# Optimization experiments

Measured on AMD Instinct MI355X. Metric: run time of the kernel, lower is better.

The kernel has to match this reference:

```python
import jax, jax.numpy as jnp
import numpy as np

EPS = 1e-7  # K.epsilon()
ROUTINGS = 3
NUM_CAPSULE = 32
DIM_CAPSULE = 64

def _squash(x, axis=-1):
    # NOTE: this repo's 'squash' is just L2-ish normalization: x / sqrt(||x||^2 + eps)
    s2 = jnp.sum(jnp.square(x), axis=axis, keepdims=True)
    return x / jnp.sqrt(s2 + EPS)

def setup_inputs() -> dict:
    key = jax.random.key(0)
    k1, k2 = jax.random.split(key)
    u_vecs = jax.random.normal(k1, (32, 1024, 256), dtype=jnp.float32)
    # shared-weight capsule kernel: (1, input_dim_capsule, num_capsule*dim_capsule)
    W = jax.random.normal(k2, (1, 256, NUM_CAPSULE * DIM_CAPSULE), dtype=jnp.float32) * 0.05
    return {"u_vecs": u_vecs, "W": W}

def reference(u_vecs, W):
    B, N, D = u_vecs.shape
    # conv1d with width-1 kernel == matmul over feature dim
    u_hat = jnp.einsum('bnd,dm->bnm', u_vecs, W[0])          # [B, N, NC*DC]
    u_hat = u_hat.reshape(B, N, NUM_CAPSULE, DIM_CAPSULE)
    u_hat = jnp.transpose(u_hat, (0, 2, 1, 3))               # [B, NC, N, DC]

    b = jnp.zeros((B, NUM_CAPSULE, N), dtype=u_hat.dtype)    # routing logits
    v = None
    for i in range(ROUTINGS):
        c = jax.nn.softmax(b, axis=-1)                       # over input capsules
        s = jnp.einsum('bij,bijd->bid', c, u_hat)            # weighted sum
        v = _squash(s)                                       # [B, NC, DC]
        if i < ROUTINGS - 1:
            b = b + jnp.einsum('bid,bijd->bij', v, u_hat)    # agreement update
    return v
```

## Files before the change

kernel.cpp:

```cpp
#include <hip/hip_runtime.h>
#include <math.h>


typedef short v8s __attribute__((ext_vector_type(8)));
typedef short v4s __attribute__((ext_vector_type(4)));
typedef float v4f __attribute__((ext_vector_type(4)));

__device__ __forceinline__ unsigned short f2bf(float x) {
    unsigned u = __float_as_uint(x);
    u = u + 0x7fffu + ((u >> 16) & 1u);
    return (unsigned short)(u >> 16);
}
__device__ __forceinline__ float bf2f(unsigned short h) {
    return __uint_as_float(((unsigned)h) << 16);
}

__global__ __launch_bounds__(256) void k_init(const float* __restrict__ U,
                                              const float* __restrict__ W,
                                              float* __restrict__ t0p,
                                              float* __restrict__ WT) {
    int bid = blockIdx.x, tid = threadIdx.x;
    if (bid < 512) {
        int b = bid >> 4, q = bid & 15;
        const float* Up = U + (((b << 10) + (q << 6)) << 8) + tid;
        float acc = 0.f;
        #pragma unroll 16
        for (int jl = 0; jl < 64; ++jl) acc += Up[jl << 8];
        t0p[(b << 12) + (q << 8) + tid] = acc * (1.0f / 1024.0f);
    } else {
        __shared__ float tile[64 * 65];
        int tix = bid - 512;
        int k0 = (tix >> 5) << 6, c0 = (tix & 31) << 6;
        int cc = tid & 63, g4 = tid >> 6;
        #pragma unroll
        for (int r = 0; r < 16; ++r) {
            int kk = (g4 << 4) + r;
            tile[kk * 65 + cc] = W[(k0 + kk) * 2048 + c0 + cc];
        }
        __syncthreads();
        int kk = tid & 63;
        #pragma unroll
        for (int r = 0; r < 16; ++r) {
            int c = (g4 << 4) + r;
            WT[(c0 + c) * 256 + k0 + kk] = tile[kk * 65 + c];
        }
    }
}

__global__ __launch_bounds__(256) void k_sv(const float* __restrict__ t0p,
                                            const float* __restrict__ tpart,
                                            const float* __restrict__ sefpart,
                                            const float* __restrict__ W,
                                            const float* __restrict__ WT,
                                            short* __restrict__ wbt_h,
                                            short* __restrict__ wbt_l,
                                            float* __restrict__ out,
                                            int mode, int writeOut) {
    __shared__ float t_lds[256];
    __shared__ float spart[256];
    __shared__ __align__(16) float v_lds[64];
    __shared__ __align__(16) v4f spartw[256];
    __shared__ float sefv_s;
    int bid = blockIdx.x, tid = threadIdx.x;
    int b = bid >> 5, iG = bid & 31;
    int bg = (b << 1) | (iG >> 4), il = iG & 15;

    float acc = 0.f;
    if (mode == 0) {
        const float* tb = t0p + (b << 12) + tid;
        #pragma unroll
        for (int q = 0; q < 16; ++q) acc += tb[q << 8];
        if (tid == 0) sefv_s = 1.0f;
    } else {
        const float* tb = tpart + (((bg << 4) + il) << 8) + tid;
        #pragma unroll
        for (int p = 0; p < 16; ++p) acc += tb[p << 18];
        if (tid == 0) {
            float s = 0.f;
            #pragma unroll
            for (int p = 0; p < 16; ++p) s += sefpart[(p << 10) + (bg << 4) + il];
            sefv_s = s;
        }
    }
    t_lds[tid] = acc;
    __syncthreads();

    int d = tid & 63, kq = tid >> 6;
    const float* Wc = W + ((kq << 6) * 2048) + (iG << 6) + d;
    float s = 0.f;
    #pragma unroll 4
    for (int kk = 0; kk < 64; ++kk)
        s += t_lds[(kq << 6) + kk] * Wc[kk * 2048];
    spart[tid] = s;
    __syncthreads();

    if (tid < 64) {
        float sv = spart[tid] + spart[tid + 64] + spart[tid + 128] + spart[tid + 192];
        float n2 = sv * sv;
        #pragma unroll
        for (int m = 1; m < 64; m <<= 1) n2 += __shfl_xor(n2, m, 64);
        float sf = sefv_s;
        float v = sv * rsqrtf(n2 + 1e-7f * sf * sf);
        v_lds[tid] = v;
        if (writeOut) out[(bid << 6) + tid] = v;
    }
    __syncthreads();
    if (writeOut) return;

    int k4 = tid & 63, dq = tid >> 6;
    const float4* WT4 = (const float4*)WT;
    v4f wp = {0.f, 0.f, 0.f, 0.f};
    #pragma unroll
    for (int dd = 0; dd < 16; ++dd) {
        float vv = v_lds[(dq << 4) + dd];
        float4 wt = WT4[((iG << 6) + (dq << 4) + dd) * 64 + k4];
        wp.x += vv * wt.x; wp.y += vv * wt.y; wp.z += vv * wt.z; wp.w += vv * wt.w;
    }
    spartw[(dq << 6) + k4] = wp;
    __syncthreads();
    if (tid < 64) {
        v4f w = spartw[tid] + spartw[64 + tid] + spartw[128 + tid] + spartw[192 + tid];
        float wv4[4] = {w.x, w.y, w.z, w.w};
        unsigned short wh[4], wl[4];
        #pragma unroll
        for (int e = 0; e < 4; ++e) {
            wh[e] = f2bf(wv4[e]);
            wl[e] = f2bf(wv4[e] - bf2f(wh[e]));
        }
        int base = (((bg << 4) + il) << 8) + (tid << 2);
        *(v4s*)&wbt_h[base] = (v4s){(short)wh[0], (short)wh[1], (short)wh[2], (short)wh[3]};
        *(v4s*)&wbt_l[base] = (v4s){(short)wl[0], (short)wl[1], (short)wl[2], (short)wl[3]};
    }
}

__global__ __launch_bounds__(1024, 8) void k_pass(const float* __restrict__ U,
                                                  const short* __restrict__ wbt_h,
                                                  const short* __restrict__ wbt_l,
                                                  float* __restrict__ bmatg,
                                                  float* __restrict__ tpart_out,
                                                  float* __restrict__ sefpart_out,
                                                  int addold) {
    __shared__ short s_U[64 * 268];
    __shared__ short s_wh[2 * 16 * 264];
    __shared__ short s_wl[2 * 16 * 264];
    __shared__ short s_eh[2 * 16 * 72];
    __shared__ short s_el[2 * 16 * 72];
    __shared__ float s_sefp[8 * 16];

    const int tid = threadIdx.x, wv = tid >> 6, lane = tid & 63;
    const int quad = lane >> 4, nn = lane & 15;
    const int blk = blockIdx.x;
    const int b = blk & 31, p = blk >> 5;
    const int rowbase = (b << 10) + (p << 6);

    {
        const float4* U4 = (const float4*)U;
        int col = tid & 63, row0 = tid >> 6;
        float4 g[4];
        #pragma unroll
        for (int q = 0; q < 4; ++q)
            g[q] = U4[(rowbase + row0 + (q << 4)) * 64 + col];
        #pragma unroll
        for (int q = 0; q < 4; ++q)
            *(v4s*)&s_U[(row0 + (q << 4)) * 268 + (col << 2)] =
                (v4s){(short)f2bf(g[q].x), (short)f2bf(g[q].y),
                      (short)f2bf(g[q].z), (short)f2bf(g[q].w)};
        int row = tid >> 5, seg = tid & 31;
        int gidx = (((b << 5) + row) << 8) + (seg << 3);
        int lidx = (row >> 4) * 4224 + (row & 15) * 264 + (seg << 3);
        *(v8s*)&s_wh[lidx] = *(const v8s*)(wbt_h + gidx);
        *(v8s*)&s_wl[lidx] = *(const v8s*)(wbt_l + gidx);
    }
    __syncthreads();

    if (wv < 8) {
        const int jt = wv & 3, g2 = wv >> 2;
        const int bg = (b << 1) | g2;
        v4f dacc = {0.f, 0.f, 0.f, 0.f};
        #pragma unroll
        for (int c = 0; c < 8; ++c) {
            int kb = (c << 5) + (quad << 3);
            v8s a  = *(const v8s*)&s_U[((jt << 4) + nn) * 268 + kb];
            v8s bh = *(const v8s*)&s_wh[g2 * 4224 + nn * 264 + kb];
            v8s bl = *(const v8s*)&s_wl[g2 * 4224 + nn * 264 + kb];
            dacc = __builtin_amdgcn_mfma_f32_16x16x32_bf16(a, bh, dacc, 0, 0, 0);
            dacc = __builtin_amdgcn_mfma_f32_16x16x32_bf16(a, bl, dacc, 0, 0, 0);
        }
        float se = 0.f;
        #pragma unroll
        for (int r = 0; r < 4; ++r) {
            int jloc = (jt << 4) + (quad << 2) + r;
            int ga = (((bg << 10) + (p << 6) + jloc) << 4) + nn;
            float val = dacc[r];
            if (addold) val += bmatg[ga];
            else bmatg[ga] = val;
            float e = __expf(val);
            unsigned short eh = f2bf(e);
            s_eh[g2 * 1152 + nn * 72 + jloc] = (short)eh;
            s_el[g2 * 1152 + nn * 72 + jloc] = (short)f2bf(e - bf2f(eh));
            se += e;
        }
        se += __shfl_xor(se, 16, 64);
        se += __shfl_xor(se, 32, 64);
        if (lane < 16) s_sefp[((g2 << 2) + jt) << 4 | lane] = se;
    }
    __syncthreads();

    {
        const int g2 = wv >> 3, kt2 = wv & 7;
        const int bg = (b << 1) | g2;
        #pragma unroll
        for (int task = 0; task < 2; ++task) {
            const int k0 = ((task << 3) + kt2) << 4;
            v4f tacc = {0.f, 0.f, 0.f, 0.f};
            #pragma unroll
            for (int jc = 0; jc < 2; ++jc) {
                v8s aeh = *(const v8s*)&s_eh[g2 * 1152 + nn * 72 + (jc << 5) + (quad << 3)];
                v8s ael = *(const v8s*)&s_el[g2 * 1152 + nn * 72 + (jc << 5) + (quad << 3)];
                short bu[8];
                #pragma unroll
                for (int jj = 0; jj < 8; ++jj)
                    bu[jj] = s_U[((jc << 5) + (quad << 3) + jj) * 268 + k0 + nn];
                v8s bf = (v8s){bu[0], bu[1], bu[2], bu[3],
                               bu[4], bu[5], bu[6], bu[7]};
                tacc = __builtin_amdgcn_mfma_f32_16x16x32_bf16(aeh, bf, tacc, 0, 0, 0);
                tacc = __builtin_amdgcn_mfma_f32_16x16x32_bf16(ael, bf, tacc, 0, 0, 0);
            }
            #pragma unroll
            for (int r = 0; r < 4; ++r) {
                int i = (quad << 2) + r;
                tpart_out[(((((p << 6) + bg) << 4) + i) << 8) + k0 + nn] = tacc[r];
            }
        }
    }
    if (tid < 32) {
        int g2 = tid >> 4, i = tid & 15;
        float ss = 0.f;
        #pragma unroll
        for (int jt = 0; jt < 4; ++jt) ss += s_sefp[((g2 << 2) + jt) << 4 | i];
        sefpart_out[(p << 10) + (((b << 1) | g2) << 4) + i] = ss;
    }
}

extern "C" void kernel_launch(void* const* d_in, const int* in_sizes, int n_in,
                              void* d_out, int out_size, void* d_ws, size_t ws_size,
                              hipStream_t stream) {
    const float* U = (const float*)d_in[0];
    const float* W = (const float*)d_in[1];
    float* out = (float*)d_out;
    float* ws = (float*)d_ws;

    float* t0p   = ws;
    float* WT    = t0p + 131072;
    float* bmatg = WT + 524288;
    float* tp    = bmatg + 1048576;
    float* sefp  = tp + 4194304;
    short* wbt_h = (short*)(sefp + 16384);
    short* wbt_l = wbt_h + 262144;

    k_init<<<640, 256, 0, stream>>>(U, W, t0p, WT);
    k_sv<<<1024, 256, 0, stream>>>(t0p, tp, sefp, W, WT,
                                   wbt_h, wbt_l, out, 0, 0);
    k_pass<<<512, 1024, 0, stream>>>(U, wbt_h, wbt_l, bmatg, tp, sefp, 0);
    k_sv<<<1024, 256, 0, stream>>>(t0p, tp, sefp, W, WT,
                                   wbt_h, wbt_l, out, 1, 0);
    k_pass<<<512, 1024, 0, stream>>>(U, wbt_h, wbt_l, bmatg, tp, sefp, 1);
    k_sv<<<1024, 256, 0, stream>>>(t0p, tp, sefp, W, WT,
                                   wbt_h, wbt_l, out, 1, 1);
}
```

Measured before the change: 133.1 us.

## Fuse init and first routing step into one kernel k_sv0d

Merges the column-mean of U, the W transpose and the first s/v/W·v computation into one kernel launched with 160 blocks of 1024 threads. The mean is folded into the first-iteration kernel, so the t0p round trip and one launch go away. The trade-off is that only 32 blocks handle the per-batch work: each one reads a full 1 MB slice of U and does a long serial k-loop over W. That leaves the device underused compared with the previous 512+1024 blocks and may lengthen this stage.

```diff
diff --git a/kernel.cpp b/kernel.cpp
--- a/kernel.cpp
+++ b/kernel.cpp
@@ -15,47 +15,111 @@
     return __uint_as_float(((unsigned)h) << 16);
 }
 
-__global__ __launch_bounds__(256) void k_init(const float* __restrict__ U,
-                                              const float* __restrict__ W,
-                                              float* __restrict__ t0p,
-                                              float* __restrict__ WT) {
-    int bid = blockIdx.x, tid = threadIdx.x;
-    if (bid < 512) {
-        int b = bid >> 4, q = bid & 15;
-        const float* Up = U + (((b << 10) + (q << 6)) << 8) + tid;
-        float acc = 0.f;
-        #pragma unroll 16
-        for (int jl = 0; jl < 64; ++jl) acc += Up[jl << 8];
-        t0p[(b << 12) + (q << 8) + tid] = acc * (1.0f / 1024.0f);
-    } else {
+__global__ __launch_bounds__(1024) void k_sv0d(const float* __restrict__ U,
+                                               const float* __restrict__ W,
+                                               float* __restrict__ WT,
+                                               short* __restrict__ wbt_h,
+                                               short* __restrict__ wbt_l) {
+    const int bid = blockIdx.x, tid = threadIdx.x;
+    if (bid >= 32) {
         __shared__ float tile[64 * 65];
-        int tix = bid - 512;
+        int tix = bid - 32;
         int k0 = (tix >> 5) << 6, c0 = (tix & 31) << 6;
-        int cc = tid & 63, g4 = tid >> 6;
-        #pragma unroll
-        for (int r = 0; r < 16; ++r) {
-            int kk = (g4 << 4) + r;
+        int cc = tid & 63, rg = tid >> 6;
+        #pragma unroll
+        for (int e = 0; e < 4; ++e) {
+            int kk = (rg << 2) + e;
             tile[kk * 65 + cc] = W[(k0 + kk) * 2048 + c0 + cc];
         }
         __syncthreads();
         int kk = tid & 63;
         #pragma unroll
-        for (int r = 0; r < 16; ++r) {
-            int c = (g4 << 4) + r;
+        for (int e = 0; e < 4; ++e) {
+            int c = (rg << 2) + e;
             WT[(c0 + c) * 256 + k0 + kk] = tile[kk * 65 + c];
         }
-    }
-}
-
-__global__ __launch_bounds__(256) void k_sv(const float* __restrict__ t0p,
-                                            const float* __restrict__ tpart,
+        return;
+    }
+    __shared__ float part[4 * 256];
+    __shared__ float t_lds[256];
+    __shared__ float v_all[32 * 64];
+    const int b = bid;
+
+    {
+        int k = tid & 255, jg = tid >> 8;
+        const float* Up = U + (b << 18) + (jg << 16) + k;
+        float acc = 0.f;
+        #pragma unroll 8
+        for (int jj = 0; jj < 256; ++jj) acc += Up[jj << 8];
+        part[(jg << 8) + k] = acc;
+    }
+    __syncthreads();
+    if (tid < 256)
+        t_lds[tid] = (part[tid] + part[256 + tid] + part[512 + tid] +
+                      part[768 + tid]) * (1.0f / 1024.0f);
+    __syncthreads();
+
+    {
+        const int lane = tid & 63, wv = tid >> 6;
+        #pragma unroll
+        for (int half = 0; half < 2; ++half) {
+            int iG = (half << 4) + wv;
+            const float* Wc = W + (iG << 6) + lane;
+            float s = 0.f;
+            #pragma unroll 4
+            for (int k = 0; k < 256; ++k) s += t_lds[k] * Wc[k * 2048];
+            float n2 = s * s;
+            #pragma unroll
+            for (int m = 1; m < 64; m <<= 1) n2 += __shfl_xor(n2, m, 64);
+            float v = s * rsqrtf(n2 + 1e-7f);
+            v_all[(iG << 6) + lane] = v;
+        }
+    }
+    __syncthreads();
+
+    {
+        int iG = tid >> 5, k8 = tid & 31;
+        int g2 = iG >> 4, il = iG & 15;
+        int bg = (b << 1) | g2;
+        const float* vv = &v_all[iG << 6];
+        const float4* W4 = (const float4*)W;
+        float wk[8];
+        #pragma unroll
+        for (int e = 0; e < 8; ++e) {
+            int k = (k8 << 3) + e;
+            const float4* Wr = W4 + k * 512 + (iG << 4);
+            float acc = 0.f;
+            #pragma unroll
+            for (int dq = 0; dq < 16; ++dq) {
+                float4 wq = Wr[dq];
+                acc += vv[(dq << 2) + 0] * wq.x + vv[(dq << 2) + 1] * wq.y +
+                       vv[(dq << 2) + 2] * wq.z + vv[(dq << 2) + 3] * wq.w;
+            }
+            wk[e] = acc;
+        }
+        short h8[8], l8[8];
+        #pragma unroll
+        for (int e = 0; e < 8; ++e) {
+            unsigned short h = f2bf(wk[e]);
+            h8[e] = (short)h;
+            l8[e] = (short)f2bf(wk[e] - bf2f(h));
+        }
+        int base = (((bg << 4) + il) << 8) + (k8 << 3);
+        *(v8s*)&wbt_h[base] = (v8s){h8[0], h8[1], h8[2], h8[3],
+                                    h8[4], h8[5], h8[6], h8[7]};
+        *(v8s*)&wbt_l[base] = (v8s){l8[0], l8[1], l8[2], l8[3],
+                                    l8[4], l8[5], l8[6], l8[7]};
+    }
+}
+
+__global__ __launch_bounds__(256) void k_sv(const float* __restrict__ tpart,
                                             const float* __restrict__ sefpart,
                                             const float* __restrict__ W,
                                             const float* __restrict__ WT,
                                             short* __restrict__ wbt_h,
                                             short* __restrict__ wbt_l,
                                             float* __restrict__ out,
-                                            int mode, int writeOut) {
+                                            int writeOut) {
     __shared__ float t_lds[256];
     __shared__ float spart[256];
     __shared__ __align__(16) float v_lds[64];
@@ -66,12 +130,7 @@
     int bg = (b << 1) | (iG >> 4), il = iG & 15;
 
     float acc = 0.f;
-    if (mode == 0) {
-        const float* tb = t0p + (b << 12) + tid;
-        #pragma unroll
-        for (int q = 0; q < 16; ++q) acc += tb[q << 8];
-        if (tid == 0) sefv_s = 1.0f;
-    } else {
+    {
         const float* tb = tpart + (((bg << 4) + il) << 8) + tid;
         #pragma unroll
         for (int p = 0; p < 16; ++p) acc += tb[p << 18];
@@ -250,21 +309,16 @@
     float* out = (float*)d_out;
     float* ws = (float*)d_ws;
 
-    float* t0p   = ws;
-    float* WT    = t0p + 131072;
+    float* WT    = ws;
     float* bmatg = WT + 524288;
     float* tp    = bmatg + 1048576;
     float* sefp  = tp + 4194304;
     short* wbt_h = (short*)(sefp + 16384);
     short* wbt_l = wbt_h + 262144;
 
-    k_init<<<640, 256, 0, stream>>>(U, W, t0p, WT);
-    k_sv<<<1024, 256, 0, stream>>>(t0p, tp, sefp, W, WT,
-                                   wbt_h, wbt_l, out, 0, 0);
+    k_sv0d<<<160, 1024, 0, stream>>>(U, W, WT, wbt_h, wbt_l);
     k_pass<<<512, 1024, 0, stream>>>(U, wbt_h, wbt_l, bmatg, tp, sefp, 0);
-    k_sv<<<1024, 256, 0, stream>>>(t0p, tp, sefp, W, WT,
-                                   wbt_h, wbt_l, out, 1, 0);
+    k_sv<<<1024, 256, 0, stream>>>(tp, sefp, W, WT, wbt_h, wbt_l, out, 0);
     k_pass<<<512, 1024, 0, stream>>>(U, wbt_h, wbt_l, bmatg, tp, sefp, 1);
-    k_sv<<<1024, 256, 0, stream>>>(t0p, tp, sefp, W, WT,
-                                   wbt_h, wbt_l, out, 1, 1);
-}
+    k_sv<<<1024, 256, 0, stream>>>(tp, sefp, W, WT, wbt_h, wbt_l, out, 1);
+}
```

Result: slower. 286.0 us (+114.8%).
